# Performance work log

Hardware: AMD Instinct MI355X
Metric: run time of the kernel (lower is better)

Reference implementation:

```python
import jax, jax.numpy as jnp
import numpy as np

B, T, D = 2, 4096, 4096
H, HKV = 32, 8
DH = D // H  # 128
EPS = 1e-5
ROPE_BASE = 10000.0


def rmsnorm(x, gamma):
    var = jnp.mean(x * x, axis=-1, keepdims=True)
    return x * jax.lax.rsqrt(var + EPS) * gamma


def rope(x):
    # x: (n, h, t, d) -- rotary applied over last dim, interleaved pairs
    d, t = x.shape[-1], x.shape[-2]
    inv_freq = 1.0 / (ROPE_BASE ** (jnp.arange(0, d, 2, dtype=jnp.float32) / d))
    ang = jnp.arange(t, dtype=jnp.float32)[:, None] * inv_freq[None, :]  # (t, d/2)
    cos, sin = jnp.cos(ang), jnp.sin(ang)
    x1, x2 = x[..., 0::2], x[..., 1::2]
    r1 = x1 * cos - x2 * sin
    r2 = x1 * sin + x2 * cos
    return jnp.stack([r1, r2], axis=-1).reshape(x.shape)


def setup_inputs() -> dict:
    key = jax.random.key(0)
    ks = jax.random.split(key, 4)
    s_in = 1.0 / np.sqrt(D)
    x = jax.random.normal(ks[0], (B, T, D), dtype=jnp.float32)
    Wq = jax.random.normal(ks[1], (D, D), dtype=jnp.float32) * s_in
    Wk = jax.random.normal(ks[2], (D, HKV * DH), dtype=jnp.float32) * s_in
    Wv = jax.random.normal(ks[3], (D, HKV * DH), dtype=jnp.float32) * s_in
    gq = jnp.ones((D,), dtype=jnp.float32)
    gk = jnp.ones((HKV * DH,), dtype=jnp.float32)
    return {"x": x, "Wq": Wq, "Wk": Wk, "Wv": Wv, "gq": gq, "gk": gk}


def reference(x, Wq, Wk, Wv, gq, gk):
    n, t, _ = x.shape
    q = rmsnorm(x @ Wq, gq)
    k = rmsnorm(x @ Wk, gk)
    v = x @ Wv
    # (n, t, h, dh) -> (n, h, t, dh)
    q = q.reshape(n, t, H, DH).transpose(0, 2, 1, 3)
    k = k.reshape(n, t, HKV, DH).transpose(0, 2, 1, 3)
    v = v.reshape(n, t, HKV, DH).transpose(0, 2, 1, 3)
    q = rope(q)
    k = rope(k)
    n_rep = H // HKV
    k = jnp.repeat(k, n_rep, axis=1)  # repeat_interleave over head dim
    v = jnp.repeat(v, n_rep, axis=1)
    return q, k, v
```

## Files before the change

### kernel.cpp

```cpp
#include <hip/hip_runtime.h>
#include <hip/hip_bf16.h>
#include <stdint.h>

#define HS     524288UL
#define KBASE  33554432UL
#define VBASE  67108864UL
#define EPSq   1e-5f

typedef unsigned short u16;
typedef unsigned int   u32;
typedef __attribute__((ext_vector_type(8))) __bf16 bf16x8;
typedef __attribute__((ext_vector_type(4))) float  f32x4;

typedef __attribute__((address_space(3))) u32* lds_u32p;
typedef const __attribute__((address_space(1))) u32* g_u32p;

__device__ __forceinline__ void g2lds16(const void* g, void* lds) {
    __builtin_amdgcn_global_load_lds((g_u32p)(uintptr_t)g, (lds_u32p)(uintptr_t)lds, 16, 0, 0);
}
__device__ __forceinline__ u16 f2bf(float f) {
    __hip_bfloat16 h = __float2bfloat16(f);
    return __builtin_bit_cast(u16, h);
}

__device__ __forceinline__ size_t wt_row_off(int n, int mode) {
    if (mode == 0) return (size_t)n * 4096;
    int c = n >> 8;
    int head = (c / 3) * 4 + (c % 3) + 1;
    return 2 * (KBASE + (size_t)head * HS) + (size_t)(n & 255) * 4096;
}

__global__ __launch_bounds__(256) void convert_x(const float4* __restrict__ x,
                                                 ushort4* __restrict__ xb) {
    int i = blockIdx.x * 256 + threadIdx.x;
    for (int g = i; g < 8388608; g += gridDim.x * 256) {
        float4 v = x[g];
        ushort4 o;
        o.x = f2bf(v.x); o.y = f2bf(v.y); o.z = f2bf(v.z); o.w = f2bf(v.w);
        xb[g] = o;
    }
}

__global__ __launch_bounds__(256) void transpose_w(
    const float* Wq, const float* Wk, const float* Wv, u16* wt, int mode)
{
    __shared__ u16 tile[64][65];
    const int n0 = blockIdx.x * 64;
    const int k0 = blockIdx.y * 64;
    const float* src; int ldn, c0;
    if (n0 < 4096)      { src = Wq; ldn = 4096; c0 = n0; }
    else if (n0 < 5120) { src = Wk; ldn = 1024; c0 = n0 - 4096; }
    else                { src = Wv; ldn = 1024; c0 = n0 - 5120; }
    const int tx = threadIdx.x & 63, ty = threadIdx.x >> 6;
#pragma unroll
    for (int r = 0; r < 16; ++r) {
        int kr = r * 4 + ty;
        tile[tx][kr] = f2bf(src[(size_t)(k0 + kr) * ldn + c0 + tx]);
    }
    __syncthreads();
#pragma unroll
    for (int r = 0; r < 16; ++r) {
        int nr = r * 4 + ty;
        wt[wt_row_off(n0 + nr, mode) + k0 + tx] = tile[nr][tx];
    }
}

#define SBAR()  do { asm volatile("" ::: "memory"); __builtin_amdgcn_s_barrier(); \
                     asm volatile("" ::: "memory"); } while (0)
#define LGKM0() asm volatile("s_waitcnt lgkmcnt(0)" ::: "memory")
#define VMC(n)  asm volatile("s_waitcnt vmcnt(" #n ")" ::: "memory")
#define CFENCE() asm volatile("" ::: "memory")

__global__ __launch_bounds__(512, 2) void gemm_qkv(
    const u16* xb, const u16* wt, float* out, int mode)
{
    __shared__ u16 Lt[2][4][8192];

    const int tid  = threadIdx.x;
    const int lane = tid & 63;
    const int wave = tid >> 6;

    const int swz = (blockIdx.x & 7) * 96 + (blockIdx.x >> 3);
    const int m0  = (swz & 31) * 256;
    const int n0  = (swz >> 5) * 256;

    const int srow  = wave * 16 + (lane >> 3);
    const int sslot = (lane & 7) ^ (lane >> 3);
    const size_t wtb = wt_row_off(n0, mode);
    const u16* p0a = xb + (size_t)(m0 + srow)       * 4096 + sslot * 8;
    const u16* p0b = xb + (size_t)(m0 + srow + 8)   * 4096 + sslot * 8;
    const u16* p1a = xb + (size_t)(m0 + 128 + srow)     * 4096 + sslot * 8;
    const u16* p1b = xb + (size_t)(m0 + 128 + srow + 8) * 4096 + sslot * 8;
    const u16* p2a = wt + wtb + (size_t)(srow)       * 4096 + sslot * 8;
    const u16* p2b = wt + wtb + (size_t)(srow + 8)   * 4096 + sslot * 8;
    const u16* p3a = wt + wtb + (size_t)(128 + srow)     * 4096 + sslot * 8;
    const u16* p3b = wt + wtb + (size_t)(128 + srow + 8) * 4096 + sslot * 8;
    const int dst0 = wave * 1024;

#define STAGE(buf, sec) do { \
    g2lds16(p##sec##a, &Lt[buf][sec][dst0]);       p##sec##a += 64; \
    g2lds16(p##sec##b, &Lt[buf][sec][dst0 + 512]); p##sec##b += 64; \
} while (0)

    const int wm = wave >> 2, wn = wave & 3;
    const int col16 = lane & 15, quad = lane >> 4;
    const int sl0 = (quad ^ (col16 & 7)) * 8;
    const int sl1 = sl0 ^ 32;

    bf16x8 a[2][4];
    bf16x8 bb[2][2][2];
    f32x4  acc[8][4];
#pragma unroll
    for (int i = 0; i < 8; ++i)
#pragma unroll
        for (int j = 0; j < 4; ++j) acc[i][j] = (f32x4)0.0f;

#define READ_A(buf, mq) do { \
    _Pragma("unroll") \
    for (int mf2 = 0; mf2 < 4; ++mf2) { \
        const u16* _p = &Lt[buf][wm][((mq) * 64 + mf2 * 16 + col16) * 64]; \
        a[0][mf2] = *(const bf16x8*)(_p + sl0); \
        a[1][mf2] = *(const bf16x8*)(_p + sl1); \
    } \
} while (0)

#define READ_B(buf, nh) do { \
    _Pragma("unroll") \
    for (int nf2 = 0; nf2 < 2; ++nf2) { \
        const u16* _p = &Lt[buf][2 + (wn >> 1)] \
                          [((wn & 1) * 64 + (nh) * 32 + nf2 * 16 + col16) * 64]; \
        bb[nh][0][nf2] = *(const bf16x8*)(_p + sl0); \
        bb[nh][1][nf2] = *(const bf16x8*)(_p + sl1); \
    } \
} while (0)

#define MMA(mq, nh) do { \
    __builtin_amdgcn_s_setprio(1); \
    _Pragma("unroll") \
    for (int mf2 = 0; mf2 < 4; ++mf2) \
    _Pragma("unroll") \
    for (int nf2 = 0; nf2 < 2; ++nf2) { \
        acc[(mq)*4+mf2][(nh)*2+nf2] = __builtin_amdgcn_mfma_f32_16x16x32_bf16( \
            a[0][mf2], bb[nh][0][nf2], acc[(mq)*4+mf2][(nh)*2+nf2], 0, 0, 0); \
        acc[(mq)*4+mf2][(nh)*2+nf2] = __builtin_amdgcn_mfma_f32_16x16x32_bf16( \
            a[1][mf2], bb[nh][1][nf2], acc[(mq)*4+mf2][(nh)*2+nf2], 0, 0, 0); \
    } \
    __builtin_amdgcn_s_setprio(0); \
} while (0)

    STAGE(0, 2); STAGE(0, 3); STAGE(0, 0); STAGE(0, 1);
    CFENCE();
    STAGE(1, 2); STAGE(1, 3); STAGE(1, 0);
    VMC(6);
    SBAR();

    for (int it = 0; it < 31; ++it) {
        READ_A(0, 0); READ_B(0, 0); STAGE(1, 1);
        SBAR(); LGKM0(); MMA(0, 0); SBAR();
        READ_B(0, 1); STAGE(0, 2);
        SBAR(); LGKM0(); MMA(0, 1); SBAR();
        READ_A(0, 1); STAGE(0, 3);
        SBAR(); LGKM0(); MMA(1, 1); SBAR();
        STAGE(0, 0);
        SBAR(); LGKM0(); MMA(1, 0); VMC(6); SBAR();
        READ_A(1, 0); READ_B(1, 0); STAGE(0, 1);
        SBAR(); LGKM0(); MMA(0, 0); SBAR();
        READ_B(1, 1); STAGE(1, 2);
        SBAR(); LGKM0(); MMA(0, 1); SBAR();
        READ_A(1, 1); STAGE(1, 3);
        SBAR(); LGKM0(); MMA(1, 1); SBAR();
        STAGE(1, 0);
        SBAR(); LGKM0(); MMA(1, 0); VMC(6); SBAR();
    }

    READ_A(0, 0); READ_B(0, 0); STAGE(1, 1);
    SBAR(); LGKM0(); MMA(0, 0); SBAR();
    READ_B(0, 1);
    SBAR(); LGKM0(); MMA(0, 1); SBAR();
    READ_A(0, 1);
    SBAR(); LGKM0(); MMA(1, 1); SBAR();
    SBAR(); LGKM0(); MMA(1, 0); VMC(0); SBAR();
    READ_A(1, 0); READ_B(1, 0);
    SBAR(); LGKM0(); MMA(0, 0); SBAR();
    READ_B(1, 1);
    SBAR(); LGKM0(); MMA(0, 1); SBAR();
    READ_A(1, 1);
    SBAR(); LGKM0(); MMA(1, 1); SBAR();
    SBAR(); LGKM0(); MMA(1, 0);

#undef STAGE
#undef READ_A
#undef READ_B
#undef MMA

    const int b_idx = m0 >> 12;
    const int tbase = m0 & 4095;
    const int ng0   = n0 + wn * 64;
    size_t headbase; int nslots = 1;
    if (ng0 < 4096) {
        headbase = (size_t)(b_idx * 32 + (ng0 >> 7)) * HS;
    } else if (ng0 < 5120) {
        headbase = KBASE + (size_t)(b_idx * 32 + ((ng0 - 4096) >> 7) * 4) * HS;
    } else {
        headbase = VBASE + (size_t)(b_idx * 32 + ((ng0 - 5120) >> 7) * 4) * HS;
        nslots = 4;
    }
    const int c0 = (ng0 & 127) + col16;
#pragma unroll
    for (int mf = 0; mf < 8; ++mf) {
#pragma unroll
        for (int r = 0; r < 4; ++r) {
            int mlocal = wm * 128 + mf * 16 + quad * 4 + r;
            size_t rowb = headbase + (size_t)(tbase + mlocal) * 128;
#pragma unroll
            for (int nf = 0; nf < 4; ++nf) {
                float val = acc[mf][nf][r];
                size_t addr = rowb + c0 + nf * 16;
                out[addr] = val;
                if (nslots == 4) {
                    out[addr + HS]     = val;
                    out[addr + 2 * HS] = val;
                    out[addr + 3 * HS] = val;
                }
            }
        }
    }
}

__global__ __launch_bounds__(256) void finalize_qk(
    float* out, const float* gq, const float* gk)
{
    const int bt = blockIdx.x;
    const int b  = bt >> 12, t = bt & 4095;
    const int tid = threadIdx.x;

    float qv[8][2], kv[2][2];
    float ssq = 0.f, ssk = 0.f;
#pragma unroll
    for (int j = 0; j < 8; ++j) {
        int p = j * 256 + tid;
        int head = p >> 6, i = p & 63;
        size_t a = (size_t)(b * 32 + head) * HS + (size_t)t * 128 + 2 * i;
        float2 u = *(const float2*)(out + a);
        qv[j][0] = u.x; qv[j][1] = u.y;
        ssq += u.x * u.x + u.y * u.y;
    }
#pragma unroll
    for (int j = 0; j < 2; ++j) {
        int p = j * 256 + tid;
        int hk = p >> 6, i = p & 63;
        size_t a = KBASE + (size_t)(b * 32 + hk * 4) * HS + (size_t)t * 128 + 2 * i;
        float2 u = *(const float2*)(out + a);
        kv[j][0] = u.x; kv[j][1] = u.y;
        ssk += u.x * u.x + u.y * u.y;
    }
#pragma unroll
    for (int off = 32; off; off >>= 1) {
        ssq += __shfl_xor(ssq, off, 64);
        ssk += __shfl_xor(ssk, off, 64);
    }
    __shared__ float red[2][4];
    if ((tid & 63) == 0) { red[0][tid >> 6] = ssq; red[1][tid >> 6] = ssk; }
    __syncthreads();
    const float sq = red[0][0] + red[0][1] + red[0][2] + red[0][3];
    const float sk = red[1][0] + red[1][1] + red[1][2] + red[1][3];
    const float qs = rsqrtf(sq * (1.f / 4096.f) + EPSq);
    const float ks = rsqrtf(sk * (1.f / 1024.f) + EPSq);
    const float tf = (float)t;
    const float LN1E4_64 = 0.14391156831f;

#pragma unroll
    for (int j = 0; j < 8; ++j) {
        int p = j * 256 + tid;
        int head = p >> 6, i = p & 63;
        float ang = tf * __expf(-(float)i * LN1E4_64);
        float s, c; sincosf(ang, &s, &c);
        float2 g = *(const float2*)(gq + head * 128 + 2 * i);
        float x1 = qv[j][0] * qs * g.x;
        float x2 = qv[j][1] * qs * g.y;
        float2 o; o.x = x1 * c - x2 * s; o.y = x1 * s + x2 * c;
        size_t a = (size_t)(b * 32 + head) * HS + (size_t)t * 128 + 2 * i;
        *(float2*)(out + a) = o;
    }
#pragma unroll
    for (int j = 0; j < 2; ++j) {
        int p = j * 256 + tid;
        int hk = p >> 6, i = p & 63;
        float ang = tf * __expf(-(float)i * LN1E4_64);
        float s, c; sincosf(ang, &s, &c);
        float2 g = *(const float2*)(gk + hk * 128 + 2 * i);
        float x1 = kv[j][0] * ks * g.x;
        float x2 = kv[j][1] * ks * g.y;
        float2 o; o.x = x1 * c - x2 * s; o.y = x1 * s + x2 * c;
        size_t a = KBASE + (size_t)(b * 32 + hk * 4) * HS + (size_t)t * 128 + 2 * i;
        *(float2*)(out + a) = o;
        *(float2*)(out + a + HS) = o;
        *(float2*)(out + a + 2 * HS) = o;
        *(float2*)(out + a + 3 * HS) = o;
    }
}

__global__ __launch_bounds__(256) void gemm_f32(
    const float* x, const float* Wq, const float* Wk, const float* Wv, float* out)
{
    __shared__ float As[16][65], Bs[16][65];
    const int m0 = blockIdx.x * 64;
    const int c0 = blockIdx.y * 64;
    const float* W; int ldn, nc0;
    if (c0 < 4096)      { W = Wq; ldn = 4096; nc0 = c0; }
    else if (c0 < 5120) { W = Wk; ldn = 1024; nc0 = c0 - 4096; }
    else                { W = Wv; ldn = 1024; nc0 = c0 - 5120; }
    const int tid = threadIdx.x, tx = tid & 15, ty = tid >> 4;
    float acc[4][4] = {};
    for (int k0 = 0; k0 < 4096; k0 += 16) {
        __syncthreads();
#pragma unroll
        for (int l = 0; l < 4; ++l) {
            int idx = l * 256 + tid;
            int m = idx >> 4, k = idx & 15;
            As[k][m] = x[(size_t)(m0 + m) * 4096 + k0 + k];
        }
#pragma unroll
        for (int l = 0; l < 4; ++l) {
            int idx = l * 256 + tid;
            int k = idx >> 6, n = idx & 63;
            Bs[k][n] = W[(size_t)(k0 + k) * ldn + nc0 + n];
        }
        __syncthreads();
#pragma unroll
        for (int k = 0; k < 16; ++k) {
            float a[4], bbv[4];
#pragma unroll
            for (int i = 0; i < 4; ++i) { a[i] = As[k][ty * 4 + i]; bbv[i] = Bs[k][tx * 4 + i]; }
#pragma unroll
            for (int i = 0; i < 4; ++i)
#pragma unroll
                for (int j = 0; j < 4; ++j) acc[i][j] += a[i] * bbv[j];
        }
    }
    const int b = m0 >> 12, tbase = m0 & 4095;
#pragma unroll
    for (int i = 0; i < 4; ++i) {
#pragma unroll
        for (int j = 0; j < 4; ++j) {
            int m = ty * 4 + i, c = c0 + tx * 4 + j;
            float v = acc[i][j];
            size_t addr; int ns = 1;
            if (c < 4096) {
                addr = (size_t)(b * 32 + (c >> 7)) * HS + (size_t)(tbase + m) * 128 + (c & 127);
            } else if (c < 5120) {
                addr = KBASE + (size_t)(b * 32 + ((c - 4096) >> 7) * 4) * HS
                     + (size_t)(tbase + m) * 128 + ((c - 4096) & 127);
            } else {
                addr = VBASE + (size_t)(b * 32 + ((c - 5120) >> 7) * 4) * HS
                     + (size_t)(tbase + m) * 128 + ((c - 5120) & 127);
                ns = 4;
            }
            out[addr] = v;
            if (ns == 4) { out[addr + HS] = v; out[addr + 2 * HS] = v; out[addr + 3 * HS] = v; }
        }
    }
}

extern "C" void kernel_launch(void* const* d_in, const int* in_sizes, int n_in,
                              void* d_out, int out_size, void* d_ws, size_t ws_size,
                              hipStream_t stream)
{
    const float* x  = (const float*)d_in[0];
    const float* Wq = (const float*)d_in[1];
    const float* Wk = (const float*)d_in[2];
    const float* Wv = (const float*)d_in[3];
    const float* gq = (const float*)d_in[4];
    const float* gk = (const float*)d_in[5];
    float* out = (float*)d_out;

    const size_t xb_bytes = 8192ULL * 4096ULL * 2ULL;
    const size_t wt_bytes = 6144ULL * 4096ULL * 2ULL;
    dim3 tb(256);

    if (ws_size >= xb_bytes) {
        u16* xb = (u16*)d_ws;
        u16* wt; int mode;
        if (ws_size >= xb_bytes + wt_bytes) { wt = (u16*)((char*)d_ws + xb_bytes); mode = 0; }
        else                                { wt = (u16*)d_out; mode = 1; }
        convert_x  <<<dim3(2048),    tb, 0, stream>>>((const float4*)x, (ushort4*)xb);
        transpose_w<<<dim3(96, 64),  tb, 0, stream>>>(Wq, Wk, Wv, wt, mode);
        gemm_qkv   <<<dim3(768), dim3(512), 0, stream>>>(xb, wt, out, mode);
    } else {
        gemm_f32   <<<dim3(128, 96), tb, 0, stream>>>(x, Wq, Wk, Wv, out);
    }
    finalize_qk<<<dim3(8192), tb, 0, stream>>>(out, gq, gk);
}
```

Before: 1.024 ms.

## Merge prep kernels, precompute RoPE table, reschedule GEMM pipeline stages

Folds the x bf16 conversion and the weight transpose into one prep launch, and has that launch also fill a cos/sin table in the workspace. finalize_qk now reads that table instead of calling sincos. The old code also recomputed the same angle for every head, which the new code avoids by computing or loading it once per thread. The GEMM main loop is reordered: it drops the explicit lgkmcnt waits, issues stages in pairs with a shallower vmcnt wait, and merges two MMA phases into one. These changes aim to cut launch overhead, transcendental work, and barrier or wait stalls, but dropping the LDS waits leaves correctness to compiler-inserted waits and changes prefetch depth.

Result: no change. 1.030 ms (+0.6%).

```diff
diff --git a/kernel.cpp b/kernel.cpp
--- a/kernel.cpp
+++ b/kernel.cpp
@@ -30,46 +30,61 @@
     return 2 * (KBASE + (size_t)head * HS) + (size_t)(n & 255) * 4096;
 }
 
-__global__ __launch_bounds__(256) void convert_x(const float4* __restrict__ x,
-                                                 ushort4* __restrict__ xb) {
-    int i = blockIdx.x * 256 + threadIdx.x;
-    for (int g = i; g < 8388608; g += gridDim.x * 256) {
-        float4 v = x[g];
-        ushort4 o;
-        o.x = f2bf(v.x); o.y = f2bf(v.y); o.z = f2bf(v.z); o.w = f2bf(v.w);
-        xb[g] = o;
-    }
-}
-
-__global__ __launch_bounds__(256) void transpose_w(
-    const float* Wq, const float* Wk, const float* Wv, u16* wt, int mode)
+__global__ __launch_bounds__(256) void prep(
+    const float4* __restrict__ x, ushort4* __restrict__ xb,
+    const float* Wq, const float* Wk, const float* Wv, u16* wt, int mode,
+    float2* tab)
 {
     __shared__ u16 tile[64][65];
-    const int n0 = blockIdx.x * 64;
-    const int k0 = blockIdx.y * 64;
-    const float* src; int ldn, c0;
-    if (n0 < 4096)      { src = Wq; ldn = 4096; c0 = n0; }
-    else if (n0 < 5120) { src = Wk; ldn = 1024; c0 = n0 - 4096; }
-    else                { src = Wv; ldn = 1024; c0 = n0 - 5120; }
-    const int tx = threadIdx.x & 63, ty = threadIdx.x >> 6;
-#pragma unroll
-    for (int r = 0; r < 16; ++r) {
-        int kr = r * 4 + ty;
-        tile[tx][kr] = f2bf(src[(size_t)(k0 + kr) * ldn + c0 + tx]);
-    }
-    __syncthreads();
-#pragma unroll
-    for (int r = 0; r < 16; ++r) {
-        int nr = r * 4 + ty;
-        wt[wt_row_off(n0 + nr, mode) + k0 + tx] = tile[nr][tx];
+    const int bx = blockIdx.x, tid = threadIdx.x;
+
+    if (bx < 2048) {
+        for (int g = bx * 256 + tid; g < 8388608; g += 2048 * 256) {
+            float4 v = x[g];
+            ushort4 o;
+            o.x = f2bf(v.x); o.y = f2bf(v.y); o.z = f2bf(v.z); o.w = f2bf(v.w);
+            xb[g] = o;
+        }
+        return;
+    }
+    if (bx < 8192) {
+        const int idx = bx - 2048;
+        const int n0 = (idx % 96) * 64;
+        const int k0 = (idx / 96) * 64;
+        const float* src; int ldn, c0;
+        if (n0 < 4096)      { src = Wq; ldn = 4096; c0 = n0; }
+        else if (n0 < 5120) { src = Wk; ldn = 1024; c0 = n0 - 4096; }
+        else                { src = Wv; ldn = 1024; c0 = n0 - 5120; }
+        const int tx = tid & 63, ty = tid >> 6;
+#pragma unroll
+        for (int r = 0; r < 16; ++r) {
+            int kr = r * 4 + ty;
+            tile[tx][kr] = f2bf(src[(size_t)(k0 + kr) * ldn + c0 + tx]);
+        }
+        __syncthreads();
+#pragma unroll
+        for (int r = 0; r < 16; ++r) {
+            int nr = r * 4 + ty;
+            wt[wt_row_off(n0 + nr, mode) + k0 + tx] = tile[nr][tx];
+        }
+        return;
+    }
+    if (!tab) return;
+    const int bx2 = bx - 8192;
+    const float LN1E4_64 = 0.14391156831f;
+#pragma unroll 4
+    for (int e = 0; e < 32; ++e) {
+        int idx = e * 8192 + bx2 * 256 + tid;
+        int t = idx >> 6, i = idx & 63;
+        float ang = (float)t * expf(-(float)i * LN1E4_64);
+        float s, c; sincosf(ang, &s, &c);
+        tab[idx] = make_float2(c, s);
     }
 }
 
 #define SBAR()  do { asm volatile("" ::: "memory"); __builtin_amdgcn_s_barrier(); \
                      asm volatile("" ::: "memory"); } while (0)
-#define LGKM0() asm volatile("s_waitcnt lgkmcnt(0)" ::: "memory")
 #define VMC(n)  asm volatile("s_waitcnt vmcnt(" #n ")" ::: "memory")
-#define CFENCE() asm volatile("" ::: "memory")
 
 __global__ __launch_bounds__(512, 2) void gemm_qkv(
     const u16* xb, const u16* wt, float* out, int mode)
@@ -117,81 +132,85 @@
 
 #define READ_A(buf, mq) do { \
     _Pragma("unroll") \
-    for (int mf2 = 0; mf2 < 4; ++mf2) { \
-        const u16* _p = &Lt[buf][wm][((mq) * 64 + mf2 * 16 + col16) * 64]; \
-        a[0][mf2] = *(const bf16x8*)(_p + sl0); \
-        a[1][mf2] = *(const bf16x8*)(_p + sl1); \
-    } \
+    for (int mf2 = 0; mf2 < 4; ++mf2) \
+        a[0][mf2] = *(const bf16x8*)(&Lt[buf][wm][((mq) * 64 + mf2 * 16 + col16) * 64 + sl0]); \
+    _Pragma("unroll") \
+    for (int mf2 = 0; mf2 < 4; ++mf2) \
+        a[1][mf2] = *(const bf16x8*)(&Lt[buf][wm][((mq) * 64 + mf2 * 16 + col16) * 64 + sl1]); \
 } while (0)
 
 #define READ_B(buf, nh) do { \
     _Pragma("unroll") \
-    for (int nf2 = 0; nf2 < 2; ++nf2) { \
-        const u16* _p = &Lt[buf][2 + (wn >> 1)] \
-                          [((wn & 1) * 64 + (nh) * 32 + nf2 * 16 + col16) * 64]; \
-        bb[nh][0][nf2] = *(const bf16x8*)(_p + sl0); \
-        bb[nh][1][nf2] = *(const bf16x8*)(_p + sl1); \
-    } \
-} while (0)
-
-#define MMA(mq, nh) do { \
+    for (int nf2 = 0; nf2 < 2; ++nf2) \
+        bb[nh][0][nf2] = *(const bf16x8*)(&Lt[buf][2 + (wn >> 1)] \
+            [((wn & 1) * 64 + (nh) * 32 + nf2 * 16 + col16) * 64 + sl0]); \
+    _Pragma("unroll") \
+    for (int nf2 = 0; nf2 < 2; ++nf2) \
+        bb[nh][1][nf2] = *(const bf16x8*)(&Lt[buf][2 + (wn >> 1)] \
+            [((wn & 1) * 64 + (nh) * 32 + nf2 * 16 + col16) * 64 + sl1]); \
+} while (0)
+
+#define MMA_KS(mq, nh, ks) do { \
+    _Pragma("unroll") \
+    for (int mf2 = 0; mf2 < 4; ++mf2) \
+    _Pragma("unroll") \
+    for (int nf2 = 0; nf2 < 2; ++nf2) \
+        acc[(mq)*4+mf2][(nh)*2+nf2] = __builtin_amdgcn_mfma_f32_16x16x32_bf16( \
+            a[ks][mf2], bb[nh][ks][nf2], acc[(mq)*4+mf2][(nh)*2+nf2], 0, 0, 0); \
+} while (0)
+
+#define MMA2(mq, nh) do { \
     __builtin_amdgcn_s_setprio(1); \
-    _Pragma("unroll") \
-    for (int mf2 = 0; mf2 < 4; ++mf2) \
-    _Pragma("unroll") \
-    for (int nf2 = 0; nf2 < 2; ++nf2) { \
-        acc[(mq)*4+mf2][(nh)*2+nf2] = __builtin_amdgcn_mfma_f32_16x16x32_bf16( \
-            a[0][mf2], bb[nh][0][nf2], acc[(mq)*4+mf2][(nh)*2+nf2], 0, 0, 0); \
-        acc[(mq)*4+mf2][(nh)*2+nf2] = __builtin_amdgcn_mfma_f32_16x16x32_bf16( \
-            a[1][mf2], bb[nh][1][nf2], acc[(mq)*4+mf2][(nh)*2+nf2], 0, 0, 0); \
-    } \
+    MMA_KS(mq, nh, 0); MMA_KS(mq, nh, 1); \
     __builtin_amdgcn_s_setprio(0); \
 } while (0)
 
+#define MMA4(mq) do { \
+    __builtin_amdgcn_s_setprio(1); \
+    MMA_KS(mq, 1, 0); MMA_KS(mq, 1, 1); \
+    MMA_KS(mq, 0, 0); MMA_KS(mq, 0, 1); \
+    __builtin_amdgcn_s_setprio(0); \
+} while (0)
+
     STAGE(0, 2); STAGE(0, 3); STAGE(0, 0); STAGE(0, 1);
-    CFENCE();
-    STAGE(1, 2); STAGE(1, 3); STAGE(1, 0);
-    VMC(6);
+    STAGE(1, 2); STAGE(1, 3);
+    VMC(4);
     SBAR();
 
     for (int it = 0; it < 31; ++it) {
-        READ_A(0, 0); READ_B(0, 0); STAGE(1, 1);
-        SBAR(); LGKM0(); MMA(0, 0); SBAR();
-        READ_B(0, 1); STAGE(0, 2);
-        SBAR(); LGKM0(); MMA(0, 1); SBAR();
-        READ_A(0, 1); STAGE(0, 3);
-        SBAR(); LGKM0(); MMA(1, 1); SBAR();
-        STAGE(0, 0);
-        SBAR(); LGKM0(); MMA(1, 0); VMC(6); SBAR();
-        READ_A(1, 0); READ_B(1, 0); STAGE(0, 1);
-        SBAR(); LGKM0(); MMA(0, 0); SBAR();
-        READ_B(1, 1); STAGE(1, 2);
-        SBAR(); LGKM0(); MMA(0, 1); SBAR();
-        READ_A(1, 1); STAGE(1, 3);
-        SBAR(); LGKM0(); MMA(1, 1); SBAR();
-        STAGE(1, 0);
-        SBAR(); LGKM0(); MMA(1, 0); VMC(6); SBAR();
-    }
-
-    READ_A(0, 0); READ_B(0, 0); STAGE(1, 1);
-    SBAR(); LGKM0(); MMA(0, 0); SBAR();
-    READ_B(0, 1);
-    SBAR(); LGKM0(); MMA(0, 1); SBAR();
+        READ_B(0, 0); READ_A(0, 0); STAGE(1, 0);
+        SBAR(); MMA2(0, 0); SBAR();
+        READ_B(0, 1); STAGE(1, 1);
+        SBAR(); MMA2(0, 1); SBAR();
+        READ_A(0, 1); STAGE(0, 2); STAGE(0, 3);
+        SBAR(); MMA4(1); VMC(4); SBAR();
+        READ_B(1, 0); READ_A(1, 0); STAGE(0, 0);
+        SBAR(); MMA2(0, 0); SBAR();
+        READ_B(1, 1); STAGE(0, 1);
+        SBAR(); MMA2(0, 1); SBAR();
+        READ_A(1, 1); STAGE(1, 2); STAGE(1, 3);
+        SBAR(); MMA4(1); VMC(4); SBAR();
+    }
+
+    READ_B(0, 0); READ_A(0, 0); STAGE(1, 0);
+    SBAR(); MMA2(0, 0); SBAR();
+    READ_B(0, 1); STAGE(1, 1);
+    SBAR(); MMA2(0, 1); SBAR();
     READ_A(0, 1);
-    SBAR(); LGKM0(); MMA(1, 1); SBAR();
-    SBAR(); LGKM0(); MMA(1, 0); VMC(0); SBAR();
-    READ_A(1, 0); READ_B(1, 0);
-    SBAR(); LGKM0(); MMA(0, 0); SBAR();
+    SBAR(); MMA4(1); VMC(0); SBAR();
+    READ_B(1, 0); READ_A(1, 0);
+    SBAR(); MMA2(0, 0); SBAR();
     READ_B(1, 1);
-    SBAR(); LGKM0(); MMA(0, 1); SBAR();
+    SBAR(); MMA2(0, 1); SBAR();
     READ_A(1, 1);
-    SBAR(); LGKM0(); MMA(1, 1); SBAR();
-    SBAR(); LGKM0(); MMA(1, 0);
+    SBAR(); MMA4(1);
 
 #undef STAGE
 #undef READ_A
 #undef READ_B
-#undef MMA
+#undef MMA_KS
+#undef MMA2
+#undef MMA4
 
     const int b_idx = m0 >> 12;
     const int tbase = m0 & 4095;
@@ -228,7 +247,7 @@
 }
 
 __global__ __launch_bounds__(256) void finalize_qk(
-    float* out, const float* gq, const float* gk)
+    float* out, const float* gq, const float* gk, const float2* __restrict__ tab)
 {
     const int bt = blockIdx.x;
     const int b  = bt >> 12, t = bt & 4095;
@@ -266,15 +285,21 @@
     const float sk = red[1][0] + red[1][1] + red[1][2] + red[1][3];
     const float qs = rsqrtf(sq * (1.f / 4096.f) + EPSq);
     const float ks = rsqrtf(sk * (1.f / 1024.f) + EPSq);
-    const float tf = (float)t;
-    const float LN1E4_64 = 0.14391156831f;
+
+    float c, s;
+    if (tab) {
+        float2 cs = tab[(size_t)t * 64 + (tid & 63)];
+        c = cs.x; s = cs.y;
+    } else {
+        const float LN1E4_64 = 0.14391156831f;
+        float ang = (float)t * __expf(-(float)(tid & 63) * LN1E4_64);
+        sincosf(ang, &s, &c);
+    }
 
 #pragma unroll
     for (int j = 0; j < 8; ++j) {
         int p = j * 256 + tid;
         int head = p >> 6, i = p & 63;
-        float ang = tf * __expf(-(float)i * LN1E4_64);
-        float s, c; sincosf(ang, &s, &c);
         float2 g = *(const float2*)(gq + head * 128 + 2 * i);
         float x1 = qv[j][0] * qs * g.x;
         float x2 = qv[j][1] * qs * g.y;
@@ -286,8 +311,6 @@
     for (int j = 0; j < 2; ++j) {
         int p = j * 256 + tid;
         int hk = p >> 6, i = p & 63;
-        float ang = tf * __expf(-(float)i * LN1E4_64);
-        float s, c; sincosf(ang, &s, &c);
         float2 g = *(const float2*)(gk + hk * 128 + 2 * i);
         float x1 = kv[j][0] * ks * g.x;
         float x2 = kv[j][1] * ks * g.y;
@@ -374,20 +397,30 @@
     const float* gk = (const float*)d_in[5];
     float* out = (float*)d_out;
 
-    const size_t xb_bytes = 8192ULL * 4096ULL * 2ULL;
-    const size_t wt_bytes = 6144ULL * 4096ULL * 2ULL;
+    const size_t xb_bytes  = 8192ULL * 4096ULL * 2ULL;
+    const size_t wt_bytes  = 6144ULL * 4096ULL * 2ULL;
+    const size_t tab_bytes = 4096ULL * 64ULL * 8ULL;
     dim3 tb(256);
 
     if (ws_size >= xb_bytes) {
         u16* xb = (u16*)d_ws;
         u16* wt; int mode;
-        if (ws_size >= xb_bytes + wt_bytes) { wt = (u16*)((char*)d_ws + xb_bytes); mode = 0; }
-        else                                { wt = (u16*)d_out; mode = 1; }
-        convert_x  <<<dim3(2048),    tb, 0, stream>>>((const float4*)x, (ushort4*)xb);
-        transpose_w<<<dim3(96, 64),  tb, 0, stream>>>(Wq, Wk, Wv, wt, mode);
+        float2* tab = nullptr;
+        if (ws_size >= xb_bytes + wt_bytes) {
+            wt = (u16*)((char*)d_ws + xb_bytes); mode = 0;
+            if (ws_size >= xb_bytes + wt_bytes + tab_bytes)
+                tab = (float2*)((char*)d_ws + xb_bytes + wt_bytes);
+        } else {
+            wt = (u16*)d_out; mode = 1;
+            if (ws_size >= xb_bytes + tab_bytes)
+                tab = (float2*)((char*)d_ws + xb_bytes);
+        }
+        prep       <<<dim3(8224), tb, 0, stream>>>((const float4*)x, (ushort4*)xb,
+                                                   Wq, Wk, Wv, wt, mode, tab);
         gemm_qkv   <<<dim3(768), dim3(512), 0, stream>>>(xb, wt, out, mode);
+        finalize_qk<<<dim3(8192), tb, 0, stream>>>(out, gq, gk, tab);
     } else {
         gemm_f32   <<<dim3(128, 96), tb, 0, stream>>>(x, Wq, Wk, Wv, out);
-    }
-    finalize_qk<<<dim3(8192), tb, 0, stream>>>(out, gq, gk);
-}
+        finalize_qk<<<dim3(8192), tb, 0, stream>>>(out, gq, gk, nullptr);
+    }
+}
```
